# Optimization experiments

Hardware: AMD Instinct MI355X
Metric: run time of the kernel (lower is better)

## Reference

```python
import jax, jax.numpy as jnp
import numpy as np

SEARCH = 7
KNN = 7
SIGMA = 1.0
CUTOFF = 1.0
NCLASSES = 20
H, W, N = 64, 2048, 131072


def _inv_gauss_flat(k, sigma):
    # matches get_gaussian_kernel: 2D gaussian on a k x k grid, normalized, then (1 - g)
    ax = np.arange(k, dtype=np.float32)
    xg = np.tile(ax, (k, 1))          # x varies along columns
    yg = xg.T
    mean = (k - 1) / 2.0
    var = sigma ** 2
    g = np.exp(-((xg - mean) ** 2 + (yg - mean) ** 2) / (2.0 * var)) / (2.0 * np.pi * var)
    g = g / g.sum()
    return (1.0 - g).reshape(-1).astype(np.float32)  # [k*k], row-major like F.unfold

_INV_GAUSS = jnp.asarray(_inv_gauss_flat(SEARCH, SIGMA))


def setup_inputs() -> dict:
    key = jax.random.key(0)
    k1, k2, k3, k4, k5 = jax.random.split(key, 5)
    proj_range = jax.random.normal(k1, (H, W), dtype=jnp.float32)  # negatives exercise the <0 -> inf path
    unproj_range = jax.random.uniform(k2, (N,), dtype=jnp.float32)
    proj_argmax = jax.random.randint(k3, (H, W), 0, NCLASSES)
    px = jax.random.randint(k4, (N,), 0, W)
    py = jax.random.randint(k5, (N,), 0, H)
    return {"proj_range": proj_range, "unproj_range": unproj_range,
            "proj_argmax": proj_argmax, "px": px, "py": py}


def reference(proj_range, unproj_range, proj_argmax, px, py):
    pad = (SEARCH - 1) // 2
    S2 = SEARCH * SEARCH
    # F.unfold flattens the kernel row-major: index i -> (dy, dx) = (i // S, i % S)
    dy = jnp.repeat(jnp.arange(SEARCH) - pad, SEARCH)   # [S2]
    dx = jnp.tile(jnp.arange(SEARCH) - pad, SEARCH)     # [S2]

    rows = py[:, None] + dy[None, :]                    # [N, S2]; zero-padded in H
    cols = (px[:, None] + dx[None, :]) % W              # circular padding in W
    valid = (rows >= 0) & (rows < H)
    rows_c = jnp.clip(rows, 0, H - 1)

    nb_range = jnp.where(valid, proj_range[rows_c, cols], 0.0)        # zero pad like F.unfold
    nb_range = jnp.where(nb_range < 0, jnp.inf, nb_range)
    center = (S2 - 1) // 2
    nb_range = nb_range.at[:, center].set(unproj_range)

    k2d = jnp.abs(nb_range - unproj_range[:, None]) * _INV_GAUSS[None, :]  # [N, S2]
    neg_vals, knn_idx = jax.lax.top_k(-k2d, KNN)        # k smallest distances
    knn_dist = -neg_vals                                # == gather(k2d, knn_idx)

    nb_arg = jnp.where(valid, proj_argmax[rows_c, cols], 0)            # zero pad -> class 0
    knn_arg = jnp.take_along_axis(nb_arg, knn_idx, axis=1)             # [N, KNN]
    if CUTOFF > 0:
        knn_arg = jnp.where(knn_dist > CUTOFF, NCLASSES, knn_arg)

    votes = jax.nn.one_hot(knn_arg, NCLASSES + 1, dtype=proj_range.dtype).sum(axis=1)  # [N, C+1]
    knn_out = jnp.argmax(votes[:, 1:-1], axis=1) + 1    # torch: votes[:, 1:-1].argmax + 1
    return knn_out
```

## Files before the change

### kernel.cpp

```cpp
#include <hip/hip_runtime.h>
#include <math.h>

#define SEARCH 7
#define PAD 3
#define S2 49
#define KNN 7
#define NCLASSES 20
#define H 64
#define W 2048
#define NPTS 131072
#define NTILES 32
#define TROWS 70
#define TCOLS 70
#define SPT 32
#define SLICE (NPTS / SPT)
#define KBLOCK 256
#define PPB 128
#define QCAP 512

#define SENTINEL_BITS 0x7FE0000000000000ull
#define CUTOFF_KEYMAX 0x4000000FE000003Full

struct InvG { float v[S2]; };

#define INSF(KEY) do {                                                  \
    double _x = (KEY);                                                  \
    double _t;                                                          \
    _t = fmin(s0, _x); _x = fmax(s0, _x); s0 = _t;                      \
    _t = fmin(s1, _x); _x = fmax(s1, _x); s1 = _t;                      \
    _t = fmin(s2, _x); _x = fmax(s2, _x); s2 = _t;                      \
    _t = fmin(s3, _x); _x = fmax(s3, _x); s3 = _t;                      \
    _t = fmin(s4, _x); _x = fmax(s4, _x); s4 = _t;                      \
    _t = fmin(s5, _x); _x = fmax(s5, _x); s5 = _t;                      \
    s6 = fmin(s6, _x);                                                  \
} while (0)

#define CAND(J, RB, DX) do {                                            \
    float nb = ftile[(RB) + (DX)];                                      \
    nb = (nb < 0.0f) ? __builtin_inff() : nb;                           \
    float d = fabsf(nb - u) * invg.v[J];                                \
    unsigned long long kb = (1ull << 62)                                \
        | ((unsigned long long)__float_as_uint(d) << 6)                 \
        | (unsigned)(J);                                                \
    INSF(__longlong_as_double((long long)kb));                          \
} while (0)

__global__ __launch_bounds__(KBLOCK, 4) void knn_kernel(
    const float* __restrict__ proj_range,
    const float* __restrict__ unproj_range,
    const int* __restrict__ proj_argmax,
    const int* __restrict__ pxv,
    const int* __restrict__ pyv,
    int* __restrict__ outv,
    InvG invg)
{
    __shared__ float  ftile[TROWS * TCOLS];
    __shared__ double kbuf[PPB][KNN];
    __shared__ unsigned queue[QCAP];
    __shared__ int qcnt;

    const int tid  = threadIdx.x;
    const int t    = blockIdx.x >> 5;
    const int sub  = blockIdx.x & 31;
    const int tbase = t << 6;
    const int lane = tid & 63;
    const int wave = tid >> 6;

    if (tid == 0) qcnt = 0;

#pragma unroll
    for (int it = 0; it < 18; ++it) {
        int r = it * 4 + wave;
        if (r < TROWS) {
            int sr = r - 3;
            bool vr = (unsigned)sr < (unsigned)H;
            int gb = (vr ? sr : 0) * W;
            int ca = (tbase - 3 + lane) & (W - 1);
            float fv = proj_range[gb + ca];
            ftile[r * TCOLS + lane] = vr ? fv : 0.0f;
            if (lane < TCOLS - 64) {
                int cb = (tbase - 3 + 64 + lane) & (W - 1);
                float fv2 = proj_range[gb + cb];
                ftile[r * TCOLS + 64 + lane] = vr ? fv2 : 0.0f;
            }
        }
    }
    __syncthreads();

    {
        const int4* px4 = (const int4*)pxv;
        int base4 = (sub * SLICE) >> 2;
#pragma unroll
        for (int k = 0; k < 4; ++k) {
            int idx4 = base4 + k * KBLOCK + tid;
            int4 v = px4[idx4];
            int i0x = idx4 * 4;
#pragma unroll
            for (int e = 0; e < 4; ++e) {
                int x = (e == 0) ? v.x : (e == 1) ? v.y : (e == 2) ? v.z : v.w;
                if ((x >> 6) == t) {
                    int i = i0x + e;
                    int y = pyv[i];
                    int pos = atomicAdd(&qcnt, 1);
                    if (pos < QCAP)
                        queue[pos] = (unsigned)i | ((unsigned)(x & 63) << 17)
                                                | ((unsigned)y << 23);
                }
            }
        }
    }
    __syncthreads();
    const int count = min(qcnt, QCAP);

    const int pairp = wave >> 1;
    const int role  = wave & 1;
    const int pidx  = pairp * 64 + lane;

    for (int base = 0; base < count; base += PPB) {
        int slot = base + pidx;
        bool active = slot < count;
        bool anyact = __ballot(active) != 0;
        unsigned pk = 0u; int i = 0, xl = 0, y = 0;

        if (anyact) {
            pk = active ? queue[slot] : 0u;
            i  = (int)(pk & 0x1FFFFu);
            xl = (int)((pk >> 17) & 63u);
            y  = (int)((pk >> 23) & 63u);
            float u = unproj_range[i];

            double s0, s1, s2, s3, s4, s5, s6;
            s0 = s1 = s2 = s3 = s4 = s5 = s6 =
                __longlong_as_double((long long)SENTINEL_BITS);

            if (role == 0) {
#pragma unroll
                for (int dy = -3; dy <= 0; ++dy) {
                    int rb = (y + dy + 3) * TCOLS + xl + 3;
                    const int dxmax = (dy == 0) ? -1 : 3;
#pragma unroll
                    for (int dx = -3; dx <= dxmax; ++dx) {
                        const int j = (dy + 3) * 7 + (dx + 3);
                        CAND(j, rb, dx);
                    }
                }
            } else {
                INSF(__longlong_as_double((long long)((1ull << 62) | 24ull)));
#pragma unroll
                for (int dy = 0; dy <= 3; ++dy) {
                    int rb = (y + dy + 3) * TCOLS + xl + 3;
                    const int dxmin = (dy == 0) ? 1 : -3;
#pragma unroll
                    for (int dx = dxmin; dx <= 3; ++dx) {
                        const int j = (dy + 3) * 7 + (dx + 3);
                        CAND(j, rb, dx);
                    }
                }
                kbuf[pidx][0] = s0; kbuf[pidx][1] = s1; kbuf[pidx][2] = s2;
                kbuf[pidx][3] = s3; kbuf[pidx][4] = s4; kbuf[pidx][5] = s5;
                kbuf[pidx][6] = s6;
            }
            if (role == 0) {
                __syncthreads();
                double m0 = fmin(s0, kbuf[pidx][6]);
                double m1 = fmin(s1, kbuf[pidx][5]);
                double m2 = fmin(s2, kbuf[pidx][4]);
                double m3 = fmin(s3, kbuf[pidx][3]);
                double m4 = fmin(s4, kbuf[pidx][2]);
                double m5 = fmin(s5, kbuf[pidx][1]);
                double m6 = fmin(s6, kbuf[pidx][0]);

                const double cutmax = __longlong_as_double((long long)CUTOFF_KEYMAX);
                int c0, c1, c2, c3, c4, c5, c6;
#define CLSK(MK, CK) do {                                                \
                long long kb = __double_as_longlong(MK);                 \
                int j = (int)(kb & 63);                                  \
                bool sel = (MK) <= cutmax;                               \
                int dy7 = (j * 37) >> 8;                                 \
                int sr = y + dy7 - 3;                                    \
                bool vrow = (unsigned)sr < (unsigned)H;                  \
                int src = min(max(sr, 0), H - 1);                        \
                int colw = (tbase - 3 + xl + (j - dy7 * 7)) & (W - 1);   \
                int cc = proj_argmax[src * W + colw];                    \
                CK = (sel && vrow) ? cc : 0;                             \
            } while (0)
                CLSK(m0, c0); CLSK(m1, c1); CLSK(m2, c2); CLSK(m3, c3);
                CLSK(m4, c4); CLSK(m5, c5); CLSK(m6, c6);
#undef CLSK

                int n0 = 1, n1 = 1, n2 = 1, n3 = 1, n4 = 1, n5 = 1, n6 = 1;
#define PAIRV(A, B) do { bool e = (c##A == c##B); n##A += e ? 1 : 0; n##B += e ? 1 : 0; } while (0)
                PAIRV(0,1); PAIRV(0,2); PAIRV(0,3); PAIRV(0,4); PAIRV(0,5); PAIRV(0,6);
                PAIRV(1,2); PAIRV(1,3); PAIRV(1,4); PAIRV(1,5); PAIRV(1,6);
                PAIRV(2,3); PAIRV(2,4); PAIRV(2,5); PAIRV(2,6);
                PAIRV(3,4); PAIRV(3,5); PAIRV(3,6);
                PAIRV(4,5); PAIRV(4,6);
                PAIRV(5,6);
#undef PAIRV

                int best = 0;
#define SCORE(K) do {                                                    \
                bool valid = (unsigned)(c##K - 1) < (unsigned)(NCLASSES - 1);\
                int sc = valid ? ((n##K << 5) | (31 - c##K)) : 0;        \
                best = max(best, sc);                                    \
            } while (0)
                SCORE(0); SCORE(1); SCORE(2); SCORE(3); SCORE(4); SCORE(5); SCORE(6);
#undef SCORE
                if (active) {
                    int res = (best == 0) ? 1 : (31 - (best & 31));
                    __builtin_nontemporal_store(res, &outv[i]);
                }
                __syncthreads();
            } else {
                __syncthreads();
                __syncthreads();
            }
        } else {
            __syncthreads();
            __syncthreads();
        }
    }
}

extern "C" void kernel_launch(void* const* d_in, const int* in_sizes, int n_in,
                              void* d_out, int out_size, void* d_ws, size_t ws_size,
                              hipStream_t stream) {
    const float* proj_range   = (const float*)d_in[0];
    const float* unproj_range = (const float*)d_in[1];
    const int*   proj_argmax  = (const int*)d_in[2];
    const int*   px           = (const int*)d_in[3];
    const int*   py           = (const int*)d_in[4];
    int* out = (int*)d_out;

    InvG invg;
    float g[S2];
    for (int yy = 0; yy < SEARCH; ++yy) {
        for (int xx = 0; xx < SEARCH; ++xx) {
            float fdx = (float)xx - 3.0f;
            float fdy = (float)yy - 3.0f;
            float s   = fdx * fdx + fdy * fdy;
            float arg = -s / 2.0f;
            float e   = (float)exp((double)arg);
            float gg  = e / 6.2831855f;
            g[yy * SEARCH + xx] = gg;
        }
    }
    float r[8];
    for (int tt = 0; tt < 8; ++tt) r[tt] = g[tt];
    int ii;
    for (ii = 8; ii + 8 <= 48; ii += 8)
        for (int tt = 0; tt < 8; ++tt) r[tt] += g[ii + tt];
    float ssum = ((r[0] + r[1]) + (r[2] + r[3])) + ((r[4] + r[5]) + (r[6] + r[7]));
    for (; ii < S2; ++ii) ssum += g[ii];
    for (int tt = 0; tt < S2; ++tt) invg.v[tt] = 1.0f - (g[tt] / ssum);

    knn_kernel<<<NTILES * SPT, KBLOCK, 0, stream>>>(
        proj_range, unproj_range, proj_argmax, px, py, out, invg);
}
```

Before: 21.03 us.

## Process each point in one thread instead of splitting candidates across wave pairs

Removes the two-wave split where each pair of waves handled half of a point's 48 neighbours and merged partial top-7 lists through shared memory. Each thread now scans all 49 candidates for its point, with no kbuf staging and no per-iteration __syncthreads. This cuts shared memory traffic and barriers and lets 256 points be in flight per block iteration instead of 128. In exchange each thread runs a serial insertion chain twice as long, which lengthens per-thread latency and reduces instruction-level parallelism.

```diff
diff --git a/kernel.cpp b/kernel.cpp
--- a/kernel.cpp
+++ b/kernel.cpp
@@ -15,7 +15,6 @@
 #define SPT 32
 #define SLICE (NPTS / SPT)
 #define KBLOCK 256
-#define PPB 128
 #define QCAP 512
 
 #define SENTINEL_BITS 0x7FE0000000000000ull
@@ -55,7 +54,6 @@
     InvG invg)
 {
     __shared__ float  ftile[TROWS * TCOLS];
-    __shared__ double kbuf[PPB][KNN];
     __shared__ unsigned queue[QCAP];
     __shared__ int qcnt;
 
@@ -112,113 +110,68 @@
     __syncthreads();
     const int count = min(qcnt, QCAP);
 
-    const int pairp = wave >> 1;
-    const int role  = wave & 1;
-    const int pidx  = pairp * 64 + lane;
-
-    for (int base = 0; base < count; base += PPB) {
-        int slot = base + pidx;
-        bool active = slot < count;
-        bool anyact = __ballot(active) != 0;
-        unsigned pk = 0u; int i = 0, xl = 0, y = 0;
-
-        if (anyact) {
-            pk = active ? queue[slot] : 0u;
-            i  = (int)(pk & 0x1FFFFu);
-            xl = (int)((pk >> 17) & 63u);
-            y  = (int)((pk >> 23) & 63u);
-            float u = unproj_range[i];
-
-            double s0, s1, s2, s3, s4, s5, s6;
-            s0 = s1 = s2 = s3 = s4 = s5 = s6 =
-                __longlong_as_double((long long)SENTINEL_BITS);
-
-            if (role == 0) {
-#pragma unroll
-                for (int dy = -3; dy <= 0; ++dy) {
-                    int rb = (y + dy + 3) * TCOLS + xl + 3;
-                    const int dxmax = (dy == 0) ? -1 : 3;
-#pragma unroll
-                    for (int dx = -3; dx <= dxmax; ++dx) {
-                        const int j = (dy + 3) * 7 + (dx + 3);
-                        CAND(j, rb, dx);
-                    }
-                }
-            } else {
-                INSF(__longlong_as_double((long long)((1ull << 62) | 24ull)));
-#pragma unroll
-                for (int dy = 0; dy <= 3; ++dy) {
-                    int rb = (y + dy + 3) * TCOLS + xl + 3;
-                    const int dxmin = (dy == 0) ? 1 : -3;
-#pragma unroll
-                    for (int dx = dxmin; dx <= 3; ++dx) {
-                        const int j = (dy + 3) * 7 + (dx + 3);
-                        CAND(j, rb, dx);
-                    }
-                }
-                kbuf[pidx][0] = s0; kbuf[pidx][1] = s1; kbuf[pidx][2] = s2;
-                kbuf[pidx][3] = s3; kbuf[pidx][4] = s4; kbuf[pidx][5] = s5;
-                kbuf[pidx][6] = s6;
+    for (int slot = tid; slot < count; slot += KBLOCK) {
+        unsigned pk = queue[slot];
+        int i  = (int)(pk & 0x1FFFFu);
+        int xl = (int)((pk >> 17) & 63u);
+        int y  = (int)((pk >> 23) & 63u);
+        float u = unproj_range[i];
+
+        const double sent = __longlong_as_double((long long)SENTINEL_BITS);
+        double s0 = sent, s1 = sent, s2 = sent, s3 = sent,
+               s4 = sent, s5 = sent, s6 = sent;
+
+        INSF(__longlong_as_double((long long)((1ull << 62) | 24ull)));
+
+#pragma unroll
+        for (int dy = -3; dy <= 3; ++dy) {
+            int rb = (y + dy + 3) * TCOLS + xl + 3;
+#pragma unroll
+            for (int dx = -3; dx <= 3; ++dx) {
+                const int j = (dy + 3) * 7 + (dx + 3);
+                if (j == 24) continue;
+                CAND(j, rb, dx);
             }
-            if (role == 0) {
-                __syncthreads();
-                double m0 = fmin(s0, kbuf[pidx][6]);
-                double m1 = fmin(s1, kbuf[pidx][5]);
-                double m2 = fmin(s2, kbuf[pidx][4]);
-                double m3 = fmin(s3, kbuf[pidx][3]);
-                double m4 = fmin(s4, kbuf[pidx][2]);
-                double m5 = fmin(s5, kbuf[pidx][1]);
-                double m6 = fmin(s6, kbuf[pidx][0]);
-
-                const double cutmax = __longlong_as_double((long long)CUTOFF_KEYMAX);
-                int c0, c1, c2, c3, c4, c5, c6;
+        }
+
+        const double cutmax = __longlong_as_double((long long)CUTOFF_KEYMAX);
+        int c0, c1, c2, c3, c4, c5, c6;
 #define CLSK(MK, CK) do {                                                \
-                long long kb = __double_as_longlong(MK);                 \
-                int j = (int)(kb & 63);                                  \
-                bool sel = (MK) <= cutmax;                               \
-                int dy7 = (j * 37) >> 8;                                 \
-                int sr = y + dy7 - 3;                                    \
-                bool vrow = (unsigned)sr < (unsigned)H;                  \
-                int src = min(max(sr, 0), H - 1);                        \
-                int colw = (tbase - 3 + xl + (j - dy7 * 7)) & (W - 1);   \
-                int cc = proj_argmax[src * W + colw];                    \
-                CK = (sel && vrow) ? cc : 0;                             \
-            } while (0)
-                CLSK(m0, c0); CLSK(m1, c1); CLSK(m2, c2); CLSK(m3, c3);
-                CLSK(m4, c4); CLSK(m5, c5); CLSK(m6, c6);
+        long long kb = __double_as_longlong(MK);                         \
+        int j = (int)(kb & 63);                                          \
+        bool sel = (MK) <= cutmax;                                       \
+        int dy7 = (j * 37) >> 8;                                         \
+        int sr = y + dy7 - 3;                                            \
+        bool vrow = (unsigned)sr < (unsigned)H;                          \
+        int src = min(max(sr, 0), H - 1);                                \
+        int colw = (tbase - 3 + xl + (j - dy7 * 7)) & (W - 1);           \
+        int cc = proj_argmax[src * W + colw];                            \
+        CK = (sel && vrow) ? cc : 0;                                     \
+    } while (0)
+        CLSK(s0, c0); CLSK(s1, c1); CLSK(s2, c2); CLSK(s3, c3);
+        CLSK(s4, c4); CLSK(s5, c5); CLSK(s6, c6);
 #undef CLSK
 
-                int n0 = 1, n1 = 1, n2 = 1, n3 = 1, n4 = 1, n5 = 1, n6 = 1;
+        int n0 = 1, n1 = 1, n2 = 1, n3 = 1, n4 = 1, n5 = 1, n6 = 1;
 #define PAIRV(A, B) do { bool e = (c##A == c##B); n##A += e ? 1 : 0; n##B += e ? 1 : 0; } while (0)
-                PAIRV(0,1); PAIRV(0,2); PAIRV(0,3); PAIRV(0,4); PAIRV(0,5); PAIRV(0,6);
-                PAIRV(1,2); PAIRV(1,3); PAIRV(1,4); PAIRV(1,5); PAIRV(1,6);
-                PAIRV(2,3); PAIRV(2,4); PAIRV(2,5); PAIRV(2,6);
-                PAIRV(3,4); PAIRV(3,5); PAIRV(3,6);
-                PAIRV(4,5); PAIRV(4,6);
-                PAIRV(5,6);
+        PAIRV(0,1); PAIRV(0,2); PAIRV(0,3); PAIRV(0,4); PAIRV(0,5); PAIRV(0,6);
+        PAIRV(1,2); PAIRV(1,3); PAIRV(1,4); PAIRV(1,5); PAIRV(1,6);
+        PAIRV(2,3); PAIRV(2,4); PAIRV(2,5); PAIRV(2,6);
+        PAIRV(3,4); PAIRV(3,5); PAIRV(3,6);
+        PAIRV(4,5); PAIRV(4,6);
+        PAIRV(5,6);
 #undef PAIRV
 
-                int best = 0;
+        int best = 0;
 #define SCORE(K) do {                                                    \
-                bool valid = (unsigned)(c##K - 1) < (unsigned)(NCLASSES - 1);\
-                int sc = valid ? ((n##K << 5) | (31 - c##K)) : 0;        \
-                best = max(best, sc);                                    \
-            } while (0)
-                SCORE(0); SCORE(1); SCORE(2); SCORE(3); SCORE(4); SCORE(5); SCORE(6);
+        bool valid = (unsigned)(c##K - 1) < (unsigned)(NCLASSES - 1);    \
+        int sc = valid ? ((n##K << 5) | (31 - c##K)) : 0;                \
+        best = max(best, sc);                                            \
+    } while (0)
+        SCORE(0); SCORE(1); SCORE(2); SCORE(3); SCORE(4); SCORE(5); SCORE(6);
 #undef SCORE
-                if (active) {
-                    int res = (best == 0) ? 1 : (31 - (best & 31));
-                    __builtin_nontemporal_store(res, &outv[i]);
-                }
-                __syncthreads();
-            } else {
-                __syncthreads();
-                __syncthreads();
-            }
-        } else {
-            __syncthreads();
-            __syncthreads();
-        }
+        int res = (best == 0) ? 1 : (31 - (best & 31));
+        __builtin_nontemporal_store(res, &outv[i]);
     }
 }
 
```

Measured after the change: 19.80 us. 1.06x faster.
